# Performance work log

Measured on AMD Instinct MI355X. Metric: run time of the kernel, lower is better.

The kernel has to match this reference:

```python
import jax, jax.numpy as jnp
import numpy as np

H, C = 8, 16           # heads, per-head channels
NEG_SLOPE = 0.2        # PyG GATConv leaky_relu slope
N_NODES, N_EDGES, F_IN, N_GRAPHS = 50000, 600000, 64, 500


def setup_inputs() -> dict:
    key = jax.random.key(0)
    ks = jax.random.split(key, 24)
    s = 0.1  # weight init scale
    inp = {
        "x": jax.random.normal(ks[0], (N_NODES, F_IN), jnp.float32),
        "edge_index": jax.random.randint(ks[1], (2, N_EDGES), 0, N_NODES, dtype=jnp.int64),
        "batch": jnp.sort(jax.random.randint(ks[2], (N_NODES,), 0, N_GRAPHS, dtype=jnp.int64)),
        "W1": jax.random.normal(ks[3], (F_IN, H * C), jnp.float32) * s,
        "as1": jax.random.normal(ks[4], (H, C), jnp.float32) * s,
        "ad1": jax.random.normal(ks[5], (H, C), jnp.float32) * s,
        "b1": jnp.zeros((H * C,), jnp.float32),
        "W2": jax.random.normal(ks[6], (H * C, H * C), jnp.float32) * s,
        "as2": jax.random.normal(ks[7], (H, C), jnp.float32) * s,
        "ad2": jax.random.normal(ks[8], (H, C), jnp.float32) * s,
        "b2": jnp.zeros((H * C,), jnp.float32),
        "W3": jax.random.normal(ks[9], (H * C, H * C), jnp.float32) * s,
        "as3": jax.random.normal(ks[10], (H, C), jnp.float32) * s,
        "ad3": jax.random.normal(ks[11], (H, C), jnp.float32) * s,
        "b3": jnp.zeros((H * C,), jnp.float32),
        "fc1_w": jax.random.normal(ks[12], (H * C, 10), jnp.float32) * s,
        "fc1_b": jnp.zeros((10,), jnp.float32),
        "fc2_w": jax.random.normal(ks[13], (10, 1), jnp.float32) * s,
        "fc2_b": jnp.zeros((1,), jnp.float32),
    }
    return inp


def gat_layer(x, src, dst, W, att_src, att_dst, bias, n):
    # x: [N, F_in] -> h: [N, H, C]
    h = (x @ W).reshape(n, H, C)
    a_src = jnp.sum(h * att_src, axis=-1)  # [N, H]
    a_dst = jnp.sum(h * att_dst, axis=-1)  # [N, H]
    e = jax.nn.leaky_relu(a_src[src] + a_dst[dst], NEG_SLOPE)  # [E, H]
    # per-destination segment softmax (numerically stable)
    m = jax.ops.segment_max(e, dst, num_segments=n)            # [N, H]
    e = jnp.exp(e - m[dst])
    z = jax.ops.segment_sum(e, dst, num_segments=n)            # [N, H]
    alpha = e / (z[dst] + 1e-16)                               # [E, H]
    out = jax.ops.segment_sum(h[src] * alpha[:, :, None], dst, num_segments=n)  # [N, H, C]
    return out.reshape(n, H * C) + bias


def reference(x, edge_index, batch, W1, as1, ad1, b1, W2, as2, ad2, b2,
              W3, as3, ad3, b3, fc1_w, fc1_b, fc2_w, fc2_b):
    n = x.shape[0]
    # PyG GATConv default add_self_loops=True
    loop = jnp.arange(n, dtype=edge_index.dtype)
    src = jnp.concatenate([edge_index[0], loop])
    dst = jnp.concatenate([edge_index[1], loop])

    x = jax.nn.relu(gat_layer(x, src, dst, W1, as1, ad1, b1, n))
    x = jax.nn.relu(gat_layer(x, src, dst, W2, as2, ad2, b2, n))
    x = jax.nn.relu(gat_layer(x, src, dst, W3, as3, ad3, b3, n))

    # global_mean_pool over graphs
    sums = jax.ops.segment_sum(x, batch, num_segments=N_GRAPHS)          # [G, 128]
    cnts = jax.ops.segment_sum(jnp.ones((n,), x.dtype), batch, num_segments=N_GRAPHS)
    pooled = sums / jnp.maximum(cnts, 1.0)[:, None]

    hdn = jax.nn.relu(pooled @ fc1_w + fc1_b)
    return hdn @ fc2_w + fc2_b  # [G, 1]
```

## Files before the change

kernel.cpp:

```cpp
#include <hip/hip_runtime.h>
#include <hip/hip_bf16.h>

#define H 8
#define C 16
#define HC 128
#define NEG_SLOPE 0.2f

__global__ void init_kernel(int* __restrict__ deg8, int n) {
    int i = blockIdx.x * 256 + threadIdx.x;
    if (i < n) deg8[i] = 0;
}

__global__ void hist8_gptr_kernel(const int* __restrict__ ei, const int* __restrict__ batch,
                                  int* __restrict__ deg8, int* __restrict__ gptr,
                                  int E, int N, int G) {
    int t = blockIdx.x * 256 + threadIdx.x;
    int* dg = deg8 + (size_t)(blockIdx.x & 7) * N;
    int e0 = t * 8;
    if (e0 + 7 < E) {
        int4 d4a = *(const int4*)(ei + E + e0);
        int4 d4b = *(const int4*)(ei + E + e0 + 4);
        atomicAdd(&dg[d4a.x], 1);
        atomicAdd(&dg[d4a.y], 1);
        atomicAdd(&dg[d4a.z], 1);
        atomicAdd(&dg[d4a.w], 1);
        atomicAdd(&dg[d4b.x], 1);
        atomicAdd(&dg[d4b.y], 1);
        atomicAdd(&dg[d4b.z], 1);
        atomicAdd(&dg[d4b.w], 1);
    } else if (e0 < E) {
        for (int j = e0; j < E; ++j) atomicAdd(&dg[ei[E + j]], 1);
    }
    int n0 = t * 8;
    if (n0 < N) {
        int prev = (n0 == 0) ? -1 : batch[n0 - 1];
        for (int j = 0; j < 8 && n0 + j < N; ++j) {
            int i = n0 + j;
            int cur = batch[i];
            if (cur != prev)
                for (int g = prev + 1; g <= cur; ++g) gptr[g] = i;
            if (i == N - 1)
                for (int g = cur + 1; g <= G; ++g) gptr[g] = N;
            prev = cur;
        }
    }
}

__global__ void scan_blk_kernel(const int* __restrict__ deg8, int* __restrict__ o,
                                int* __restrict__ p, int n) {
    __shared__ int sh[256];
    int tid = threadIdx.x;
    int base = blockIdx.x * 1024 + tid * 4;
    int4 v = make_int4(1, 1, 1, 1);
    if (base + 3 < n) {
#pragma unroll
        for (int c = 0; c < 8; ++c) {
            int4 t4 = *(const int4*)(deg8 + (size_t)c * n + base);
            v.x += t4.x; v.y += t4.y; v.z += t4.z; v.w += t4.w;
        }
    } else {
        v = make_int4(0, 0, 0, 0);
        for (int j = 0; j < 4; ++j) {
            if (base + j < n) {
                int s = 1;
#pragma unroll
                for (int c = 0; c < 8; ++c) s += deg8[(size_t)c * n + base + j];
                (&v.x)[j] = s;
            }
        }
    }
    v.x = (v.x + 7) & ~7; v.y = (v.y + 7) & ~7;
    v.z = (v.z + 7) & ~7; v.w = (v.w + 7) & ~7;
    if (base >= n)     v.x = 0;
    if (base + 1 >= n) v.y = 0;
    if (base + 2 >= n) v.z = 0;
    if (base + 3 >= n) v.w = 0;
    int s = v.x + v.y + v.z + v.w;
    sh[tid] = s;
    __syncthreads();
    for (int off = 1; off < 256; off <<= 1) {
        int t = (tid >= off) ? sh[tid - off] : 0;
        __syncthreads();
        sh[tid] += t;
        __syncthreads();
    }
    int excl = sh[tid] - s;
    int4 ov;
    ov.x = excl; ov.y = ov.x + v.x; ov.z = ov.y + v.y; ov.w = ov.z + v.z;
    if (base + 3 < n) *(int4*)(o + base) = ov;
    else {
        if (base < n)     o[base] = ov.x;
        if (base + 1 < n) o[base + 1] = ov.y;
        if (base + 2 < n) o[base + 2] = ov.z;
        if (base + 3 < n) o[base + 3] = ov.w;
    }
    if (tid == 255) p[blockIdx.x] = sh[255];
}

__global__ void scan_part_kernel(int* __restrict__ p, int* __restrict__ tot, int nb) {
    __shared__ int sh[256];
    int tid = threadIdx.x;
    int v = (tid < nb) ? p[tid] : 0;
    sh[tid] = v;
    __syncthreads();
    for (int off = 1; off < 256; off <<= 1) {
        int t = (tid >= off) ? sh[tid - off] : 0;
        __syncthreads();
        sh[tid] += t;
        __syncthreads();
    }
    if (tid < nb) p[tid] = sh[tid] - v;
    if (tid == 255) *tot = sh[255];
}

__global__ void scan_add_kernel(int* __restrict__ o, const int* __restrict__ p, int n) {
    int off = p[blockIdx.x];
    int base = blockIdx.x * 1024 + threadIdx.x * 4;
    if (base + 3 < n) {
        int4 v = *(const int4*)(o + base);
        v.x += off; v.y += off; v.z += off; v.w += off;
        *(int4*)(o + base) = v;
    } else {
        if (base < n)     o[base] += off;
        if (base + 1 < n) o[base + 1] += off;
        if (base + 2 < n) o[base + 2] += off;
        if (base + 3 < n) o[base + 3] += off;
    }
}

__global__ void base_fill_kernel(int* __restrict__ deg8 ,
                                 const int* __restrict__ rowptr, int* __restrict__ csr, int N) {
    int d = blockIdx.x * 256 + threadIdx.x;
    if (d >= N) return;
    int base = rowptr[d];
    csr[base] = d;
    int run = base + 1;
    int cnt[8];
#pragma unroll
    for (int c = 0; c < 8; ++c) cnt[c] = deg8[(size_t)c * N + d];
#pragma unroll
    for (int c = 0; c < 8; ++c) { deg8[(size_t)c * N + d] = run; run += cnt[c]; }
    int rend = rowptr[d + 1];
    for (int p = run; p < rend; ++p) csr[p] = N;
    if (d == 0) {
        int tot = rowptr[N];
        for (int k = 0; k < 64; ++k) csr[tot + k] = N;
    }
}

__global__ void scatter8_kernel(const int* __restrict__ ei, int* __restrict__ base8,
                                int* __restrict__ csr, int E, int N) {
    int t = blockIdx.x * 256 + threadIdx.x;
    int* cur = base8 + (size_t)(blockIdx.x & 7) * N;
    int e0 = t * 8;
    if (e0 + 7 < E) {
        int4 s4a = *(const int4*)(ei + e0);
        int4 s4b = *(const int4*)(ei + e0 + 4);
        int4 d4a = *(const int4*)(ei + E + e0);
        int4 d4b = *(const int4*)(ei + E + e0 + 4);
        int p;
        p = atomicAdd(&cur[d4a.x], 1); csr[p] = s4a.x;
        p = atomicAdd(&cur[d4a.y], 1); csr[p] = s4a.y;
        p = atomicAdd(&cur[d4a.z], 1); csr[p] = s4a.z;
        p = atomicAdd(&cur[d4a.w], 1); csr[p] = s4a.w;
        p = atomicAdd(&cur[d4b.x], 1); csr[p] = s4b.x;
        p = atomicAdd(&cur[d4b.y], 1); csr[p] = s4b.y;
        p = atomicAdd(&cur[d4b.z], 1); csr[p] = s4b.z;
        p = atomicAdd(&cur[d4b.w], 1); csr[p] = s4b.w;
    } else if (e0 < E) {
        for (int j = e0; j < E; ++j) {
            int p = atomicAdd(&cur[ei[E + j]], 1);
            csr[p] = ei[j];
        }
    }
}

template <int K>
__global__ void gemm_att_kernel(const float* __restrict__ x, const float* __restrict__ W,
                                const float* __restrict__ as_, const float* __restrict__ ad_,
                                float* __restrict__ h, float* __restrict__ asrc,
                                float* __restrict__ adst, int n) {
    const int ROWS = 64;
    __shared__ float xs[ROWS][HC];
    __shared__ float wsh[2][8][HC];
    int tx = threadIdx.x & 31;
    int ty = threadIdx.x >> 5;
    int row0 = blockIdx.x * ROWS;
    int wrow = threadIdx.x >> 5;
    int wcol = (threadIdx.x & 31) * 4;

    if (blockIdx.x == 0) {
        if (threadIdx.x < HC) h[(size_t)n * HC + threadIdx.x] = 0.f;
        if (threadIdx.x < H)  asrc[(size_t)n * H + threadIdx.x] = -INFINITY;
    }

    const int NV = ROWS * K / 4;
    for (int idx = threadIdx.x; idx < NV; idx += 256) {
        int rr = idx / (K / 4), kk = idx % (K / 4);
        int gr = row0 + rr;
        float4 v = (gr < n) ? ((const float4*)(x + (size_t)gr * K))[kk]
                            : make_float4(0.f, 0.f, 0.f, 0.f);
        *(float4*)(&xs[rr][kk * 4]) = v;
    }
    *(float4*)&wsh[0][wrow][wcol] = *(const float4*)(W + (size_t)wrow * HC + wcol);
    __syncthreads();

    float acc[8][4];
#pragma unroll
    for (int r = 0; r < 8; ++r)
#pragma unroll
        for (int c = 0; c < 4; ++c) acc[r][c] = 0.f;

    const int NCH = K / 8;
    for (int c = 0; c < NCH; ++c) {
        int cur = c & 1;
        if (c + 1 < NCH)
            *(float4*)&wsh[cur ^ 1][wrow][wcol] =
                *(const float4*)(W + (size_t)((c + 1) * 8 + wrow) * HC + wcol);
#pragma unroll
        for (int k2 = 0; k2 < 2; ++k2) {
            float4 wv[4];
#pragma unroll
            for (int kk = 0; kk < 4; ++kk)
                wv[kk] = *(const float4*)&wsh[cur][k2 * 4 + kk][tx * 4];
            int kx = c * 8 + k2 * 4;
#pragma unroll
            for (int r = 0; r < 8; ++r) {
                float4 xr = *(const float4*)(&xs[ty * 8 + r][kx]);
                acc[r][0] = fmaf(xr.x, wv[0].x, acc[r][0]);
                acc[r][1] = fmaf(xr.x, wv[0].y, acc[r][1]);
                acc[r][2] = fmaf(xr.x, wv[0].z, acc[r][2]);
                acc[r][3] = fmaf(xr.x, wv[0].w, acc[r][3]);
                acc[r][0] = fmaf(xr.y, wv[1].x, acc[r][0]);
                acc[r][1] = fmaf(xr.y, wv[1].y, acc[r][1]);
                acc[r][2] = fmaf(xr.y, wv[1].z, acc[r][2]);
                acc[r][3] = fmaf(xr.y, wv[1].w, acc[r][3]);
                acc[r][0] = fmaf(xr.z, wv[2].x, acc[r][0]);
                acc[r][1] = fmaf(xr.z, wv[2].y, acc[r][1]);
                acc[r][2] = fmaf(xr.z, wv[2].z, acc[r][2]);
                acc[r][3] = fmaf(xr.z, wv[2].w, acc[r][3]);
                acc[r][0] = fmaf(xr.w, wv[3].x, acc[r][0]);
                acc[r][1] = fmaf(xr.w, wv[3].y, acc[r][1]);
                acc[r][2] = fmaf(xr.w, wv[3].z, acc[r][2]);
                acc[r][3] = fmaf(xr.w, wv[3].w, acc[r][3]);
            }
        }
        __syncthreads();
    }
#pragma unroll
    for (int r = 0; r < 8; ++r) {
        float4 o = make_float4(acc[r][0], acc[r][1], acc[r][2], acc[r][3]);
        *(float4*)(&xs[ty * 8 + r][tx * 4]) = o;
        int row = row0 + ty * 8 + r;
        if (row < n) *(float4*)(h + (size_t)row * HC + tx * 4) = o;
    }
    __syncthreads();

#pragma unroll
    for (int rep = 0; rep < 2; ++rep) {
        int pidx = threadIdx.x + rep * 256;
        int row = pidx >> 3;
        int hd = pidx & 7;
        if (row0 + row < n) {
            const float4* hv = (const float4*)&xs[row][hd * 16];
            const float4* sv = (const float4*)(as_ + hd * 16);
            const float4* dv = (const float4*)(ad_ + hd * 16);
            float s = 0.f, d = 0.f;
#pragma unroll
            for (int j = 0; j < 4; ++j) {
                float4 a = hv[j], u = sv[j], v = dv[j];
                s += a.x * u.x + a.y * u.y + a.z * u.z + a.w * u.w;
                d += a.x * v.x + a.y * v.y + a.z * v.z + a.w * v.w;
            }
            asrc[(size_t)(row0 + row) * H + hd] = s;
            adst[(size_t)(row0 + row) * H + hd] = d;
        }
    }
}

__global__ void gat_agg_kernel(const int* __restrict__ rowptr, const int* __restrict__ csr_src,
                               const float* __restrict__ h, const float* __restrict__ asrc,
                               const float* __restrict__ adst, const float* __restrict__ bias,
                               float* __restrict__ out, int N) {
    int dst = (blockIdx.x * 256 + threadIdx.x) >> 6;
    if (dst >= N) return;
    int lane = threadIdx.x & 63;
    int hd = lane >> 3;
    int beg = rowptr[dst], end = rowptr[dst + 1];
    float ad = adst[(size_t)dst * H + hd];
    const float2* h2 = (const float2*)h;

    float z = 0.f, a0 = 0.f, a1 = 0.f;
    int i0, i1, i2, i3, i4, i5, i6, i7;
    float e0, e1, e2, e3, e4, e5, e6, e7;
    float2 v0, v1, v2, v3, v4, v5, v6, v7;

#define LOADI(S, J) i##S = csr_src[(J)];
#define LOADV(S)                                                           \
    { e##S = asrc[(size_t)i##S * H + hd]; v##S = h2[(size_t)i##S * 64 + lane]; }
#define PROCE(S)                                                           \
    {   float e = e##S + ad;                                               \
        e = e > 0.f ? e : NEG_SLOPE * e;                                   \
        float w = __expf(e);                                               \
        z += w;                                                            \
        a0 = fmaf(w, v##S.x, a0);                                          \
        a1 = fmaf(w, v##S.y, a1);                                          \
    }
    LOADI(0, beg)     LOADI(1, beg + 1) LOADI(2, beg + 2) LOADI(3, beg + 3)
    LOADI(4, beg + 4) LOADI(5, beg + 5) LOADI(6, beg + 6) LOADI(7, beg + 7)
    LOADV(0) LOADV(1) LOADV(2) LOADV(3) LOADV(4) LOADV(5) LOADV(6) LOADV(7)
    LOADI(0, beg + 8)  LOADI(1, beg + 9)  LOADI(2, beg + 10) LOADI(3, beg + 11)
    LOADI(4, beg + 12) LOADI(5, beg + 13) LOADI(6, beg + 14) LOADI(7, beg + 15)

    for (int j = beg; j < end; j += 8) {
        PROCE(0) LOADV(0)
        PROCE(1) LOADV(1)
        PROCE(2) LOADV(2)
        PROCE(3) LOADV(3)
        PROCE(4) LOADV(4)
        PROCE(5) LOADV(5)
        PROCE(6) LOADV(6)
        PROCE(7) LOADV(7)
        LOADI(0, j + 16) LOADI(1, j + 17) LOADI(2, j + 18) LOADI(3, j + 19)
        LOADI(4, j + 20) LOADI(5, j + 21) LOADI(6, j + 22) LOADI(7, j + 23)
    }
#undef LOADI
#undef LOADV
#undef PROCE
    float inv = 1.f / (z + 1e-16f);
    int c2 = lane * 2;
    float r0 = fmaxf(a0 * inv + bias[c2], 0.f);
    float r1 = fmaxf(a1 * inv + bias[c2 + 1], 0.f);
    *(float2*)(out + (size_t)dst * HC + c2) = make_float2(r0, r1);
}

__global__ void pool_mlp_kernel(const float* __restrict__ x, const int* __restrict__ gptr,
                                const float* __restrict__ fc1w, const float* __restrict__ fc1b,
                                const float* __restrict__ fc2w, const float* __restrict__ fc2b,
                                float* __restrict__ out, int G) {
    __shared__ float sp[HC];
    __shared__ float sh[10];
    int g = blockIdx.x;
    int c = threadIdx.x;
    int beg = gptr[g], end = gptr[g + 1];
    float acc = 0.f;
    for (int n = beg; n < end; ++n) acc += x[(size_t)n * HC + c];
    sp[c] = acc / fmaxf((float)(end - beg), 1.f);
    __syncthreads();
    if (c < 10) {
        float s = fc1b[c];
        for (int k = 0; k < HC; ++k) s = fmaf(sp[k], fc1w[k * 10 + c], s);
        sh[c] = fmaxf(s, 0.f);
    }
    __syncthreads();
    if (c == 0) {
        float o = fc2b[0];
#pragma unroll
        for (int j = 0; j < 10; ++j) o = fmaf(sh[j], fc2w[j], o);
        out[g] = o;
    }
}

extern "C" void kernel_launch(void* const* d_in, const int* in_sizes, int n_in,
                              void* d_out, int out_size, void* d_ws, size_t ws_size,
                              hipStream_t stream) {
    const int N = in_sizes[0] / 64;
    const int E = in_sizes[1] / 2;
    const int G = out_size;
    const int CSR_CAP = E + 8 * N + 64;

    const float* x     = (const float*)d_in[0];
    const int*   ei    = (const int*)d_in[1];
    const int*   batch = (const int*)d_in[2];
    const float* W1 = (const float*)d_in[3];
    const float* as1 = (const float*)d_in[4];
    const float* ad1 = (const float*)d_in[5];
    const float* b1 = (const float*)d_in[6];
    const float* W2 = (const float*)d_in[7];
    const float* as2 = (const float*)d_in[8];
    const float* ad2 = (const float*)d_in[9];
    const float* b2 = (const float*)d_in[10];
    const float* W3 = (const float*)d_in[11];
    const float* as3 = (const float*)d_in[12];
    const float* ad3 = (const float*)d_in[13];
    const float* b3 = (const float*)d_in[14];
    const float* fc1w = (const float*)d_in[15];
    const float* fc1b = (const float*)d_in[16];
    const float* fc2w = (const float*)d_in[17];
    const float* fc2b = (const float*)d_in[18];

    float* ws = (float*)d_ws;
    float* h    = ws;
    float* xb0  = h + (size_t)(N + 1) * HC;
    float* xb1  = xb0 + (size_t)N * HC;
    float* asrc = xb1 + (size_t)N * HC;
    float* adst = asrc + (size_t)(N + 1) * H;
    int* ints   = (int*)(adst + (size_t)N * H);
    int* deg8   = ints;
    int* rowptr = deg8 + (size_t)8 * N;
    int* gptr   = rowptr + N + 16;
    int* partN  = gptr + G + 16;
    int* csr    = partN + 256;

    dim3 blk(256);
    int grid8   = ((E + 7) / 8 + 255) / 256;
    int grid_n  = (N + 255) / 256;
    int grid_agg = (N * 64 + 255) / 256;
    int nbN = (N + 1023) / 1024;

    init_kernel<<<(8 * N + 255) / 256, blk, 0, stream>>>(deg8, 8 * N);
    hist8_gptr_kernel<<<grid8, blk, 0, stream>>>(ei, batch, deg8, gptr, E, N, G);
    scan_blk_kernel<<<nbN, blk, 0, stream>>>(deg8, rowptr, partN, N);
    scan_part_kernel<<<1, blk, 0, stream>>>(partN, rowptr + N, nbN);
    scan_add_kernel<<<nbN, blk, 0, stream>>>(rowptr, partN, N);
    base_fill_kernel<<<grid_n, blk, 0, stream>>>(deg8, rowptr, csr, N);
    scatter8_kernel<<<grid8, blk, 0, stream>>>(ei, deg8, csr, E, N);

    auto run_layer = [&](const float* xin, int K, const float* W, const float* as_,
                         const float* ad_, const float* b, float* out) {
        if (K == 64)
            gemm_att_kernel<64><<<(N + 63) / 64, blk, 0, stream>>>(xin, W, as_, ad_,
                                                                   h, asrc, adst, N);
        else
            gemm_att_kernel<128><<<(N + 63) / 64, blk, 0, stream>>>(xin, W, as_, ad_,
                                                                    h, asrc, adst, N);
        gat_agg_kernel<<<grid_agg, blk, 0, stream>>>(rowptr, csr, h, asrc, adst, b, out, N);
    };

    run_layer(x,   64,  W1, as1, ad1, b1, xb0);
    run_layer(xb0, 128, W2, as2, ad2, b2, xb1);
    run_layer(xb1, 128, W3, as3, ad3, b3, xb0);

    pool_mlp_kernel<<<G, dim3(128), 0, stream>>>(xb0, gptr, fc1w, fc1b, fc2w, fc2b,
                                                 (float*)d_out, G);
}
```

Measured before the change: 362.5 us.

## Fuse CSR scan finalize kernels and vectorize neighbor index loads

Merges scan_part, scan_add and base_fill into a single finalize kernel. Each block re-scans the block partials itself and then writes row pointers, CSR base offsets and padding in one pass. The init kernel is replaced with hipMemsetAsync. In the aggregation kernel, the eight per-neighbor index loads become two int4 loads, relying on row starts padded to multiples of 8. This cuts launch count and scalar index traffic, at the cost of every block redundantly scanning the partials.

```diff
diff --git a/kernel.cpp b/kernel.cpp
--- a/kernel.cpp
+++ b/kernel.cpp
@@ -5,11 +5,6 @@
 #define C 16
 #define HC 128
 #define NEG_SLOPE 0.2f
-
-__global__ void init_kernel(int* __restrict__ deg8, int n) {
-    int i = blockIdx.x * 256 + threadIdx.x;
-    if (i < n) deg8[i] = 0;
-}
 
 __global__ void hist8_gptr_kernel(const int* __restrict__ ei, const int* __restrict__ batch,
                                   int* __restrict__ deg8, int* __restrict__ gptr,
@@ -97,10 +92,12 @@
     if (tid == 255) p[blockIdx.x] = sh[255];
 }
 
-__global__ void scan_part_kernel(int* __restrict__ p, int* __restrict__ tot, int nb) {
+__global__ void finalize_kernel(int* __restrict__ rowptr ,
+                                const int* __restrict__ partials, int nb,
+                                int* __restrict__ deg8, int* __restrict__ csr, int N) {
     __shared__ int sh[256];
     int tid = threadIdx.x;
-    int v = (tid < nb) ? p[tid] : 0;
+    int v = (tid < nb) ? partials[tid] : 0;
     sh[tid] = v;
     __syncthreads();
     for (int off = 1; off < 256; off <<= 1) {
@@ -109,42 +106,29 @@
         sh[tid] += t;
         __syncthreads();
     }
-    if (tid < nb) p[tid] = sh[tid] - v;
-    if (tid == 255) *tot = sh[255];
-}
-
-__global__ void scan_add_kernel(int* __restrict__ o, const int* __restrict__ p, int n) {
-    int off = p[blockIdx.x];
-    int base = blockIdx.x * 1024 + threadIdx.x * 4;
-    if (base + 3 < n) {
-        int4 v = *(const int4*)(o + base);
-        v.x += off; v.y += off; v.z += off; v.w += off;
-        *(int4*)(o + base) = v;
-    } else {
-        if (base < n)     o[base] += off;
-        if (base + 1 < n) o[base + 1] += off;
-        if (base + 2 < n) o[base + 2] += off;
-        if (base + 3 < n) o[base + 3] += off;
-    }
-}
-
-__global__ void base_fill_kernel(int* __restrict__ deg8 ,
-                                 const int* __restrict__ rowptr, int* __restrict__ csr, int N) {
-    int d = blockIdx.x * 256 + threadIdx.x;
-    if (d >= N) return;
-    int base = rowptr[d];
-    csr[base] = d;
-    int run = base + 1;
-    int cnt[8];
-#pragma unroll
-    for (int c = 0; c < 8; ++c) cnt[c] = deg8[(size_t)c * N + d];
-#pragma unroll
-    for (int c = 0; c < 8; ++c) { deg8[(size_t)c * N + d] = run; run += cnt[c]; }
-    int rend = rowptr[d + 1];
-    for (int p = run; p < rend; ++p) csr[p] = N;
-    if (d == 0) {
-        int tot = rowptr[N];
-        for (int k = 0; k < 64; ++k) csr[tot + k] = N;
+    int carry = (blockIdx.x > 0) ? sh[blockIdx.x - 1] : 0;
+    int base = blockIdx.x * 1024 + tid * 4;
+#pragma unroll
+    for (int j = 0; j < 4; ++j) {
+        int d = base + j;
+        if (d >= N) break;
+        int rp = rowptr[d] + carry;
+        rowptr[d] = rp;
+        int cnt[8];
+        int s = 1;
+#pragma unroll
+        for (int c = 0; c < 8; ++c) { cnt[c] = deg8[(size_t)c * N + d]; s += cnt[c]; }
+        int pad = (s + 7) & ~7;
+        csr[rp] = d;
+        int run = rp + 1;
+#pragma unroll
+        for (int c = 0; c < 8; ++c) { deg8[(size_t)c * N + d] = run; run += cnt[c]; }
+        int rend = rp + pad;
+        for (int p = run; p < rend; ++p) csr[p] = N;
+        if (d == N - 1) {
+            rowptr[N] = rend;
+            for (int k = 0; k < 64; ++k) csr[rend + k] = N;
+        }
     }
 }
 
@@ -295,7 +279,11 @@
     float e0, e1, e2, e3, e4, e5, e6, e7;
     float2 v0, v1, v2, v3, v4, v5, v6, v7;
 
-#define LOADI(S, J) i##S = csr_src[(J)];
+#define LOADI_G(B)                                                         \
+    { int4 ia = *(const int4*)(csr_src + (B));                             \
+      int4 ib = *(const int4*)(csr_src + (B) + 4);                         \
+      i0 = ia.x; i1 = ia.y; i2 = ia.z; i3 = ia.w;                          \
+      i4 = ib.x; i5 = ib.y; i6 = ib.z; i7 = ib.w; }
 #define LOADV(S)                                                           \
     { e##S = asrc[(size_t)i##S * H + hd]; v##S = h2[(size_t)i##S * 64 + lane]; }
 #define PROCE(S)                                                           \
@@ -306,11 +294,9 @@
         a0 = fmaf(w, v##S.x, a0);                                          \
         a1 = fmaf(w, v##S.y, a1);                                          \
     }
-    LOADI(0, beg)     LOADI(1, beg + 1) LOADI(2, beg + 2) LOADI(3, beg + 3)
-    LOADI(4, beg + 4) LOADI(5, beg + 5) LOADI(6, beg + 6) LOADI(7, beg + 7)
+    LOADI_G(beg)
     LOADV(0) LOADV(1) LOADV(2) LOADV(3) LOADV(4) LOADV(5) LOADV(6) LOADV(7)
-    LOADI(0, beg + 8)  LOADI(1, beg + 9)  LOADI(2, beg + 10) LOADI(3, beg + 11)
-    LOADI(4, beg + 12) LOADI(5, beg + 13) LOADI(6, beg + 14) LOADI(7, beg + 15)
+    LOADI_G(beg + 8)
 
     for (int j = beg; j < end; j += 8) {
         PROCE(0) LOADV(0)
@@ -321,10 +307,9 @@
         PROCE(5) LOADV(5)
         PROCE(6) LOADV(6)
         PROCE(7) LOADV(7)
-        LOADI(0, j + 16) LOADI(1, j + 17) LOADI(2, j + 18) LOADI(3, j + 19)
-        LOADI(4, j + 20) LOADI(5, j + 21) LOADI(6, j + 22) LOADI(7, j + 23)
-    }
-#undef LOADI
+        LOADI_G(j + 16)
+    }
+#undef LOADI_G
 #undef LOADV
 #undef PROCE
     float inv = 1.f / (z + 1e-16f);
@@ -404,16 +389,13 @@
 
     dim3 blk(256);
     int grid8   = ((E + 7) / 8 + 255) / 256;
-    int grid_n  = (N + 255) / 256;
     int grid_agg = (N * 64 + 255) / 256;
     int nbN = (N + 1023) / 1024;
 
-    init_kernel<<<(8 * N + 255) / 256, blk, 0, stream>>>(deg8, 8 * N);
+    hipMemsetAsync(deg8, 0, (size_t)8 * N * sizeof(int), stream);
     hist8_gptr_kernel<<<grid8, blk, 0, stream>>>(ei, batch, deg8, gptr, E, N, G);
     scan_blk_kernel<<<nbN, blk, 0, stream>>>(deg8, rowptr, partN, N);
-    scan_part_kernel<<<1, blk, 0, stream>>>(partN, rowptr + N, nbN);
-    scan_add_kernel<<<nbN, blk, 0, stream>>>(rowptr, partN, N);
-    base_fill_kernel<<<grid_n, blk, 0, stream>>>(deg8, rowptr, csr, N);
+    finalize_kernel<<<nbN, blk, 0, stream>>>(rowptr, partN, nbN, deg8, csr, N);
     scatter8_kernel<<<grid8, blk, 0, stream>>>(ei, deg8, csr, E, N);
 
     auto run_layer = [&](const float* xin, int K, const float* W, const float* as_,
```

Measured after the change: 365.1 us. Within noise of the previous version (+0.7%).
